# Performance work log

Measured on AMD Instinct MI355X. Metric: run time of the kernel, lower is better.

## Reference

```python
import jax, jax.numpy as jnp
import numpy as np

NS = 0.4      # neighborhood_size
GS = 8        # grid_size
RNN = 128     # rnn_size
EMB = 64      # embedding_size
NMIX = 20     # nmixtures
N = 1024      # num pedestrians


def setup_inputs() -> dict:
    key = jax.random.key(0)
    ks = jax.random.split(key, 14)
    s = 0.05
    return {
        "xoff": jax.random.normal(ks[0], (N, 2)) * s,
        "xabs": jax.random.uniform(ks[1], (N, 2)),
        "h0": jax.random.normal(ks[2], (1, N, RNN)) * 0.1,
        "c0": jax.random.normal(ks[3], (1, N, RNN)) * 0.1,
        "W_emb": jax.random.normal(ks[4], (EMB, 2)) * s,
        "b_emb": jax.random.normal(ks[5], (EMB,)) * s,
        "W_soc": jax.random.normal(ks[6], (EMB, GS * GS * RNN)) * s,
        "b_soc": jax.random.normal(ks[7], (EMB,)) * s,
        "W_ih": jax.random.normal(ks[8], (4 * RNN, 2 * EMB)) * s,
        "W_hh": jax.random.normal(ks[9], (4 * RNN, RNN)) * s,
        "b_ih": jax.random.normal(ks[10], (4 * RNN,)) * s,
        "b_hh": jax.random.normal(ks[11], (4 * RNN,)) * s,
        "W_out": jax.random.normal(ks[12], (6 * NMIX, RNN)) * s,
        "b_out": jax.random.normal(ks[13], (6 * NMIX,)) * s,
    }


def grid_mask(xabs, dtype):
    # Vectorized getGridMask: [N, N, GS*GS] one-hot neighbor binning.
    x, y = xabs[:, 0], xabs[:, 1]
    dx = x[None, :] - (x[:, None] - NS / 2)  # other_x - width_low, [N, N]
    dy = y[None, :] - (y[:, None] - NS / 2)
    cx = jnp.floor(dx / NS * GS).astype(jnp.int32)
    cy = jnp.floor(dy / NS * GS).astype(jnp.int32)
    n = x.shape[0]
    valid = ((dx >= 0) & (dx < NS) & (dy >= 0) & (dy < NS)
             & (cx >= 0) & (cx < GS) & (cy >= 0) & (cy < GS)
             & ~jnp.eye(n, dtype=bool))
    cell = jnp.clip(cx + cy * GS, 0, GS * GS - 1)
    return jax.nn.one_hot(cell, GS * GS, dtype=dtype) * valid[..., None].astype(dtype)


def reference(xoff, xabs, h0, c0, W_emb, b_emb, W_soc, b_soc,
              W_ih, W_hh, b_ih, b_hh, W_out, b_out):
    n = xabs.shape[0]
    # predict_distance=True -> embed offsets
    emb = jax.nn.relu(xoff @ W_emb.T + b_emb)                 # [N, 64]
    grid = grid_mask(xabs, emb.dtype)                          # [N, N, 64]
    h = h0[0]                                                  # [N, 128]
    # getSocialTensor: scatter neighbor hidden states into grid bins
    social = jnp.einsum('nmg,mh->ngh', grid, h).reshape(n, GS * GS * RNN)
    pool = jax.nn.relu(social @ W_soc.T + b_soc)               # [N, 64]
    xin = jnp.concatenate([emb, pool], axis=-1)                # [N, 128]
    # single-step LSTM, torch gate order i, f, g, o
    gates = xin @ W_ih.T + h @ W_hh.T + b_ih + b_hh            # [N, 512]
    i, f, g, o = jnp.split(gates, 4, axis=-1)
    c = jax.nn.sigmoid(f) * c0[0] + jax.nn.sigmoid(i) * jnp.tanh(g)
    hn = jax.nn.sigmoid(o) * jnp.tanh(c)
    out = hn @ W_out.T + b_out                                 # [N, 120]
    mu1, mu2, ls1, ls2, rho, pi_logits = jnp.split(out, 6, axis=1)
    return (mu1, mu2, ls1, ls2, rho, pi_logits)
```

## Files before the change

### kernel.cpp

```cpp
#include <hip/hip_runtime.h>
#include <hip/hip_bf16.h>

#define NN_ 1024

#define U_WGF  0
#define U_SHI  131072
#define U_ACTH 655360
#define U_P    917504
#define F_WOUT 2555904
#define F_HN   2572288

typedef __attribute__((ext_vector_type(8))) short short8;
typedef __attribute__((ext_vector_type(4))) float floatx4;

__device__ __forceinline__ float b2f_(unsigned short u) {
    return __uint_as_float(((unsigned)u) << 16);
}
__device__ __forceinline__ unsigned short f2bu(float f) {
    __hip_bfloat16 b = __float2bfloat16(f);
    return *(unsigned short*)&b;
}
__device__ __forceinline__ float ldin(const void* p, int i, int isbf) {
    return isbf ? b2f_(((const unsigned short*)p)[i]) : ((const float*)p)[i];
}
__device__ __forceinline__ int detect_bf16(const void* Wih, int tid) {
    unsigned wv = ((const unsigned*)Wih)[tid];
    unsigned e8 = (wv >> 7) & 0xFFu;
    return (__syncthreads_count((e8 >= 96u && e8 <= 134u) ? 1 : 0) > 128) ? 1 : 0;
}

__global__ __launch_bounds__(256) void prep_kernel(
        const void* __restrict__ xoff, const void* __restrict__ h0,
        const void* __restrict__ Wsoc, const void* __restrict__ Wemb,
        const void* __restrict__ bemb, const void* __restrict__ Wih,
        const void* __restrict__ Whh,  const void* __restrict__ Wout,
        float* __restrict__ ws) {
    const int tid = threadIdx.x;
    const int isbf = detect_bf16(Wih, tid);
    unsigned short* u = (unsigned short*)ws;
    const int t0 = (blockIdx.x * 256 + tid) * 8;
    unsigned short hv[8];
    if (t0 < 131072) {
        int jl = (t0 >> 3) & 15, q = (t0 >> 7) & 3, kb = (t0 >> 9) & 7, jt = t0 >> 12;
        int j = (jt & 3) * 128 + (jt >> 2) * 16 + jl;
        int k0 = kb * 32 + q * 8;
#pragma unroll
        for (int r = 0; r < 8; r++) {
            int k = k0 + r;
            float v = (k < 128) ? ldin(Wih, j * 128 + k, isbf)
                                : ldin(Whh, j * 128 + (k - 128), isbf);
            hv[r] = f2bu(v);
        }
        *(short8*)(u + U_WGF + t0) = *(short8*)hv;
    } else if (t0 < 147456) {
        int t2 = t0 - 131072; int r = t2 >> 7, j0 = t2 & 127;
#pragma unroll
        for (int i = 0; i < 8; i++) {
            int j = j0 + i;
            ws[F_WOUT + t2 + i] = (j < 120) ? ldin(Wout, j * 128 + r, isbf) : 0.0f;
        }
    } else if (t0 < 671744) {
        int t2 = t0 - 147456;
        int e = (t2 >> 3) & 63, q = (t2 >> 9) & 3, j = (t2 >> 11) & 3, g = t2 >> 13;
        int src = e * 8192 + g * 128 + j * 32 + q * 8;
#pragma unroll
        for (int r = 0; r < 8; r++) hv[r] = f2bu(ldin(Wsoc, src + r, isbf));
        *(short8*)(u + U_SHI + t2) = *(short8*)hv;
    } else if (t0 < 802816) {
        int t2 = t0 - 671744; int n = t2 >> 7, k = t2 & 127;
#pragma unroll
        for (int i = 0; i < 8; i++) hv[i] = f2bu(ldin(h0, t2 + i, isbf));
        *(short8*)(u + U_ACTH + n * 256 + 128 + k) = *(short8*)hv;
    } else {
        int t2 = t0 - 802816; int n = t2 >> 6, e0 = t2 & 63;
        float x0 = ldin(xoff, 2 * n, isbf), x1 = ldin(xoff, 2 * n + 1, isbf);
#pragma unroll
        for (int i = 0; i < 8; i++) {
            int e = e0 + i;
            float v = fmaf(x0, ldin(Wemb, 2 * e, isbf),
                      fmaf(x1, ldin(Wemb, 2 * e + 1, isbf), ldin(bemb, e, isbf)));
            hv[i] = f2bu(fmaxf(v, 0.0f));
        }
        *(short8*)(u + U_ACTH + n * 256 + e0) = *(short8*)hv;
    }
}

__global__ __launch_bounds__(256) void pgemm_kernel(float* __restrict__ ws) {
    const unsigned short* u = (const unsigned short*)ws;
    const short* Ah  = (const short*)(u + U_ACTH);
    const short* Shi = (const short*)(u + U_SHI);
    unsigned short* P16 = (unsigned short*)ws + U_P;
    const int tid = threadIdx.x, lane = tid & 63, wv = tid >> 6;
    const int B_ = blockIdx.y * 64 + blockIdx.x;
    const int mtile = B_ & 63, rest = B_ >> 6;
    const int cg = rest >> 1, thalf = rest & 1;
    const int m = lane & 15, q = lane >> 4;
    const int g = cg * 4 + wv;
    const int abase = (mtile * 16 + m) * 256 + 128 + q * 8;
    short8 ah[4];
#pragma unroll
    for (int j = 0; j < 4; j++) ah[j] = *(const short8*)(Ah + abase + 32 * j);
    const int rowl = mtile * 16 + q * 4;
#pragma unroll
    for (int tt = 0; tt < 2; tt++) {
        const int t = thalf * 2 + tt;
        const int e = t * 16 + m;
        floatx4 c = {0.0f, 0.0f, 0.0f, 0.0f};
#pragma unroll
        for (int j = 0; j < 4; j++) {
            short8 bh = *(const short8*)(Shi + ((g * 4 + j) * 4 + q) * 512 + e * 8);
            c = __builtin_amdgcn_mfma_f32_16x16x32_bf16(ah[j], bh, c, 0, 0, 0);
        }
        const int n0 = cg * 256 + wv * 64 + t * 16;
#pragma unroll
        for (int r = 0; r < 4; r++)
            P16[(rowl + r) * 4096 + n0 + m] = f2bu(c[r]);
    }
}

__global__ __launch_bounds__(256) void pool_kernel(const void* __restrict__ xabs,
                                                   const void* __restrict__ b_soc,
                                                   const void* __restrict__ Wih_det,
                                                   float* __restrict__ ws) {
    __shared__ float xabs_s[2048];
    __shared__ int   off[NN_];
    __shared__ int   cnt_s;
    __shared__ float4 red4[16][16];
    const int tid = threadIdx.x;
    const int isbf = detect_bf16(Wih_det, tid);
    const int n = blockIdx.x;
    unsigned short* u = (unsigned short*)ws;

    for (int i = tid; i < 2048; i += 256) xabs_s[i] = ldin(xabs, i, isbf);
    if (tid == 0) cnt_s = 0;
    __syncthreads();
    {
        float xs = xabs_s[2 * n]     - 0.2f;
        float ys = xabs_s[2 * n + 1] - 0.2f;
        for (int i = tid; i < NN_; i += 256) {
            float dx = xabs_s[2 * i]     - xs;
            float dy = xabs_s[2 * i + 1] - ys;
            int cx = (int)floorf(dx / 0.4f * 8.0f);
            int cy = (int)floorf(dy / 0.4f * 8.0f);
            bool valid = (dx >= 0.0f) && (dx < 0.4f) && (dy >= 0.0f) && (dy < 0.4f)
                      && (cx >= 0) && (cx < 8) && (cy >= 0) && (cy < 8) && (i != n);
            if (valid) {
                int idx = atomicAdd(&cnt_s, 1);
                off[idx] = i * 4096 + ((cy * 8 + cx) << 6);
            }
        }
    }
    __syncthreads();
    {
        const unsigned short* P16 = (const unsigned short*)ws + U_P;
        const int strm = tid >> 4, e4 = tid & 15;
        const int cc = cnt_s;
        float ax = 0.0f, ay = 0.0f, az = 0.0f, aw = 0.0f;
        for (int j = strm; j < cc; j += 16) {
            int o = off[j];
            ushort4 uu = *(const ushort4*)(P16 + o + 4 * e4);
            ax += b2f_(uu.x); ay += b2f_(uu.y); az += b2f_(uu.z); aw += b2f_(uu.w);
        }
        red4[strm][e4] = make_float4(ax, ay, az, aw);
    }
    __syncthreads();
    if (tid < 16) {
        float s[4] = {0.0f, 0.0f, 0.0f, 0.0f};
#pragma unroll
        for (int s16 = 0; s16 < 16; s16++) {
            float4 r = red4[s16][tid];
            s[0] += r.x; s[1] += r.y; s[2] += r.z; s[3] += r.w;
        }
        int e = 4 * tid;
#pragma unroll
        for (int i = 0; i < 4; i++) {
            float v = fmaxf(s[i] + ldin(b_soc, e + i, isbf), 0.0f);
            u[U_ACTH + n * 256 + 64 + e + i] = f2bu(v);
        }
    }
}

__global__ __launch_bounds__(256) void gates_kernel(const void* __restrict__ c0,
                                                    const void* __restrict__ b_ih,
                                                    const void* __restrict__ b_hh,
                                                    const void* __restrict__ Wih_det,
                                                    float* __restrict__ ws) {
    __shared__ float gl[16][68];
    const int tid = threadIdx.x;
    const int isbf = detect_bf16(Wih_det, tid);
    const unsigned short* u = (const unsigned short*)ws;
    const short* Ah = (const short*)(u + U_ACTH);
    const short* Wg = (const short*)(u + U_WGF);
    const int lane = tid & 63, wv = tid >> 6, m = lane & 15, q = lane >> 4;
    const int m0 = blockIdx.x * 16, y = blockIdx.y;
    const int jt = y * 4 + wv;
    floatx4 acc = {0.0f, 0.0f, 0.0f, 0.0f};
#pragma unroll
    for (int kb = 0; kb < 8; kb++) {
        short8 ah = *(const short8*)(Ah + (m0 + m) * 256 + kb * 32 + q * 8);
        short8 b  = *(const short8*)(Wg + (jt * 8 + kb) * 512 + q * 128 + m * 8);
        acc = __builtin_amdgcn_mfma_f32_16x16x32_bf16(ah, b, acc, 0, 0, 0);
    }
    const int jorig = wv * 128 + y * 16 + m;
    const float bias = ldin(b_ih, jorig, isbf) + ldin(b_hh, jorig, isbf);
#pragma unroll
    for (int r = 0; r < 4; r++)
        gl[q * 4 + r][wv * 16 + m] = acc[r] + bias;
    __syncthreads();
    {
        const int a = tid >> 4, rl = tid & 15;
        const int n = m0 + a, rg = y * 16 + rl;
        float iv = gl[a][rl],      fv = gl[a][16 + rl];
        float gv = gl[a][32 + rl], ov = gl[a][48 + rl];
        float si = 1.0f / (1.0f + expf(-iv));
        float sf = 1.0f / (1.0f + expf(-fv));
        float so = 1.0f / (1.0f + expf(-ov));
        float cc = sf * ldin(c0, n * 128 + rg, isbf) + si * tanhf(gv);
        ws[F_HN + n * 128 + rg] = so * tanhf(cc);
    }
}

__global__ __launch_bounds__(256) void pwout_kernel(const void* __restrict__ b_out,
                                                    const void* __restrict__ Wih_det,
                                                    const float* __restrict__ ws,
                                                    float* __restrict__ out) {
    __shared__ __align__(16) float hnl[2][128];
    const int tid = threadIdx.x;
    const int isbf = detect_bf16(Wih_det, tid);
    const int n0 = blockIdx.x * 2;
    const int half = tid >> 7, t2 = tid & 127;
    const int n = n0 + half;
    hnl[half][t2] = ws[F_HN + n * 128 + t2];
    __syncthreads();
    if (t2 < 120) {
        int j = t2;
        float acc = ldin(b_out, j, isbf);
        for (int r = 0; r < 128; r += 4) {
            float4 hq = *(const float4*)&hnl[half][r];
            acc = fmaf(hq.x, ws[F_WOUT + (r + 0) * 128 + j], acc);
            acc = fmaf(hq.y, ws[F_WOUT + (r + 1) * 128 + j], acc);
            acc = fmaf(hq.z, ws[F_WOUT + (r + 2) * 128 + j], acc);
            acc = fmaf(hq.w, ws[F_WOUT + (r + 3) * 128 + j], acc);
        }
        int ch = j / 20, wc = j - ch * 20;
        out[ch * 20480 + n * 20 + wc] = acc;
    }
}

extern "C" void kernel_launch(void* const* d_in, const int* in_sizes, int n_in,
                              void* d_out, int out_size, void* d_ws, size_t ws_size,
                              hipStream_t stream) {
    const void* xoff  = d_in[0];
    const void* xabs  = d_in[1];
    const void* h0    = d_in[2];
    const void* c0    = d_in[3];
    const void* W_emb = d_in[4];
    const void* b_emb = d_in[5];
    const void* W_soc = d_in[6];
    const void* b_soc = d_in[7];
    const void* W_ih  = d_in[8];
    const void* W_hh  = d_in[9];
    const void* b_ih  = d_in[10];
    const void* b_hh  = d_in[11];
    const void* W_out = d_in[12];
    const void* b_out = d_in[13];
    float* ws = (float*)d_ws;
    float* out = (float*)d_out;

    prep_kernel<<<424, 256, 0, stream>>>(xoff, h0, W_soc, W_emb, b_emb,
                                         W_ih, W_hh, W_out, ws);
    pgemm_kernel<<<dim3(64, 32), 256, 0, stream>>>(ws);
    pool_kernel<<<1024, 256, 0, stream>>>(xabs, b_soc, W_ih, ws);
    gates_kernel<<<dim3(64, 8), 256, 0, stream>>>(c0, b_ih, b_hh, W_ih, ws);
    pwout_kernel<<<512, 256, 0, stream>>>(b_out, W_ih, ws, out);
}
```

Measured before the change: 117.9 us.

## Move neighbor binning into prep kernel and fuse gates with output projection

Neighbor-list construction (grid binning of xabs) moves out of pool_kernel into extra blocks of prep_kernel, which write per-pedestrian offset lists and counts to the workspace. pool_kernel then only loads the precomputed list and does the gather-reduce. gates_kernel and pwout_kernel are merged into one gateout_kernel that computes all 512 gates for 8 rows per block, applies the LSTM cell in shared memory and does the output projection, removing one launch and the hn round trip through global memory. The fused kernel wastes half of each MFMA tile, since only 8 of 16 rows are used, and runs only 128 blocks, which may underfill the GPU.

New measurement: 145.8 us. 1.24x slower.

```diff
diff --git a/kernel.cpp b/kernel.cpp
--- a/kernel.cpp
+++ b/kernel.cpp
@@ -8,7 +8,8 @@
 #define U_ACTH 655360
 #define U_P    917504
 #define F_WOUT 2555904
-#define F_HN   2572288
+#define I_OFF  2572288
+#define I_CNT  3620864
 
 typedef __attribute__((ext_vector_type(8))) short short8;
 typedef __attribute__((ext_vector_type(4))) float floatx4;
@@ -30,58 +31,88 @@
 }
 
 __global__ __launch_bounds__(256) void prep_kernel(
-        const void* __restrict__ xoff, const void* __restrict__ h0,
+        const void* __restrict__ xoff, const void* __restrict__ xabs,
+        const void* __restrict__ h0,
         const void* __restrict__ Wsoc, const void* __restrict__ Wemb,
         const void* __restrict__ bemb, const void* __restrict__ Wih,
         const void* __restrict__ Whh,  const void* __restrict__ Wout,
         float* __restrict__ ws) {
     const int tid = threadIdx.x;
+    const int bid = blockIdx.x;
     const int isbf = detect_bf16(Wih, tid);
     unsigned short* u = (unsigned short*)ws;
-    const int t0 = (blockIdx.x * 256 + tid) * 8;
-    unsigned short hv[8];
-    if (t0 < 131072) {
-        int jl = (t0 >> 3) & 15, q = (t0 >> 7) & 3, kb = (t0 >> 9) & 7, jt = t0 >> 12;
-        int j = (jt & 3) * 128 + (jt >> 2) * 16 + jl;
-        int k0 = kb * 32 + q * 8;
-#pragma unroll
-        for (int r = 0; r < 8; r++) {
-            int k = k0 + r;
-            float v = (k < 128) ? ldin(Wih, j * 128 + k, isbf)
-                                : ldin(Whh, j * 128 + (k - 128), isbf);
-            hv[r] = f2bu(v);
-        }
-        *(short8*)(u + U_WGF + t0) = *(short8*)hv;
-    } else if (t0 < 147456) {
-        int t2 = t0 - 131072; int r = t2 >> 7, j0 = t2 & 127;
-#pragma unroll
-        for (int i = 0; i < 8; i++) {
-            int j = j0 + i;
-            ws[F_WOUT + t2 + i] = (j < 120) ? ldin(Wout, j * 128 + r, isbf) : 0.0f;
-        }
-    } else if (t0 < 671744) {
-        int t2 = t0 - 147456;
-        int e = (t2 >> 3) & 63, q = (t2 >> 9) & 3, j = (t2 >> 11) & 3, g = t2 >> 13;
-        int src = e * 8192 + g * 128 + j * 32 + q * 8;
-#pragma unroll
-        for (int r = 0; r < 8; r++) hv[r] = f2bu(ldin(Wsoc, src + r, isbf));
-        *(short8*)(u + U_SHI + t2) = *(short8*)hv;
-    } else if (t0 < 802816) {
-        int t2 = t0 - 671744; int n = t2 >> 7, k = t2 & 127;
-#pragma unroll
-        for (int i = 0; i < 8; i++) hv[i] = f2bu(ldin(h0, t2 + i, isbf));
-        *(short8*)(u + U_ACTH + n * 256 + 128 + k) = *(short8*)hv;
+
+    if (bid < 424) {
+        const int t0 = (bid * 256 + tid) * 8;
+        unsigned short hv[8];
+        if (t0 < 131072) {
+            int jl = (t0 >> 3) & 15, q = (t0 >> 7) & 3, kb = (t0 >> 9) & 7, jt = t0 >> 12;
+            int j = (jt & 3) * 128 + (jt >> 2) * 16 + jl;
+            int k0 = kb * 32 + q * 8;
+#pragma unroll
+            for (int r = 0; r < 8; r++) {
+                int k = k0 + r;
+                float v = (k < 128) ? ldin(Wih, j * 128 + k, isbf)
+                                    : ldin(Whh, j * 128 + (k - 128), isbf);
+                hv[r] = f2bu(v);
+            }
+            *(short8*)(u + U_WGF + t0) = *(short8*)hv;
+        } else if (t0 < 147456) {
+            int t2 = t0 - 131072; int r = t2 >> 7, j0 = t2 & 127;
+#pragma unroll
+            for (int i = 0; i < 8; i++) {
+                int j = j0 + i;
+                ws[F_WOUT + t2 + i] = (j < 120) ? ldin(Wout, j * 128 + r, isbf) : 0.0f;
+            }
+        } else if (t0 < 671744) {
+            int t2 = t0 - 147456;
+            int e = (t2 >> 3) & 63, q = (t2 >> 9) & 3, j = (t2 >> 11) & 3, g = t2 >> 13;
+            int src = e * 8192 + g * 128 + j * 32 + q * 8;
+#pragma unroll
+            for (int r = 0; r < 8; r++) hv[r] = f2bu(ldin(Wsoc, src + r, isbf));
+            *(short8*)(u + U_SHI + t2) = *(short8*)hv;
+        } else if (t0 < 802816) {
+            int t2 = t0 - 671744; int n = t2 >> 7, k = t2 & 127;
+#pragma unroll
+            for (int i = 0; i < 8; i++) hv[i] = f2bu(ldin(h0, t2 + i, isbf));
+            *(short8*)(u + U_ACTH + n * 256 + 128 + k) = *(short8*)hv;
+        } else {
+            int t2 = t0 - 802816; int n = t2 >> 6, e0 = t2 & 63;
+            float x0 = ldin(xoff, 2 * n, isbf), x1 = ldin(xoff, 2 * n + 1, isbf);
+#pragma unroll
+            for (int i = 0; i < 8; i++) {
+                int e = e0 + i;
+                float v = fmaf(x0, ldin(Wemb, 2 * e, isbf),
+                          fmaf(x1, ldin(Wemb, 2 * e + 1, isbf), ldin(bemb, e, isbf)));
+                hv[i] = f2bu(fmaxf(v, 0.0f));
+            }
+            *(short8*)(u + U_ACTH + n * 256 + e0) = *(short8*)hv;
+        }
     } else {
-        int t2 = t0 - 802816; int n = t2 >> 6, e0 = t2 & 63;
-        float x0 = ldin(xoff, 2 * n, isbf), x1 = ldin(xoff, 2 * n + 1, isbf);
-#pragma unroll
-        for (int i = 0; i < 8; i++) {
-            int e = e0 + i;
-            float v = fmaf(x0, ldin(Wemb, 2 * e, isbf),
-                      fmaf(x1, ldin(Wemb, 2 * e + 1, isbf), ldin(bemb, e, isbf)));
-            hv[i] = f2bu(fmaxf(v, 0.0f));
-        }
-        *(short8*)(u + U_ACTH + n * 256 + e0) = *(short8*)hv;
+        __shared__ float xs_[2048];
+        __shared__ int cnt_s[4];
+        for (int i = tid; i < 2048; i += 256) xs_[i] = ldin(xabs, i, isbf);
+        if (tid < 4) cnt_s[tid] = 0;
+        __syncthreads();
+        const int a = tid >> 6, t = tid & 63;
+        const int n = (bid - 424) * 4 + a;
+        unsigned* OFF = (unsigned*)ws + I_OFF + n * 1024;
+        const float xsn = xs_[2 * n]     - 0.2f;
+        const float ysn = xs_[2 * n + 1] - 0.2f;
+        for (int i = t; i < NN_; i += 64) {
+            float dx = xs_[2 * i]     - xsn;
+            float dy = xs_[2 * i + 1] - ysn;
+            int cx = (int)floorf(dx / 0.4f * 8.0f);
+            int cy = (int)floorf(dy / 0.4f * 8.0f);
+            bool valid = (dx >= 0.0f) && (dx < 0.4f) && (dy >= 0.0f) && (dy < 0.4f)
+                      && (cx >= 0) && (cx < 8) && (cy >= 0) && (cy < 8) && (i != n);
+            if (valid) {
+                int pos = atomicAdd(&cnt_s[a], 1);
+                OFF[pos] = (unsigned)(i * 4096 + ((cy * 8 + cx) << 6));
+            }
+        }
+        __syncthreads();
+        if (tid < 4) ((unsigned*)ws)[I_CNT + (bid - 424) * 4 + tid] = (unsigned)cnt_s[tid];
     }
 }
 
@@ -118,46 +149,27 @@
     }
 }
 
-__global__ __launch_bounds__(256) void pool_kernel(const void* __restrict__ xabs,
-                                                   const void* __restrict__ b_soc,
+__global__ __launch_bounds__(256) void pool_kernel(const void* __restrict__ b_soc,
                                                    const void* __restrict__ Wih_det,
                                                    float* __restrict__ ws) {
-    __shared__ float xabs_s[2048];
-    __shared__ int   off[NN_];
-    __shared__ int   cnt_s;
+    __shared__ int off_s[1024];
     __shared__ float4 red4[16][16];
     const int tid = threadIdx.x;
     const int isbf = detect_bf16(Wih_det, tid);
     const int n = blockIdx.x;
     unsigned short* u = (unsigned short*)ws;
-
-    for (int i = tid; i < 2048; i += 256) xabs_s[i] = ldin(xabs, i, isbf);
-    if (tid == 0) cnt_s = 0;
-    __syncthreads();
-    {
-        float xs = xabs_s[2 * n]     - 0.2f;
-        float ys = xabs_s[2 * n + 1] - 0.2f;
-        for (int i = tid; i < NN_; i += 256) {
-            float dx = xabs_s[2 * i]     - xs;
-            float dy = xabs_s[2 * i + 1] - ys;
-            int cx = (int)floorf(dx / 0.4f * 8.0f);
-            int cy = (int)floorf(dy / 0.4f * 8.0f);
-            bool valid = (dx >= 0.0f) && (dx < 0.4f) && (dy >= 0.0f) && (dy < 0.4f)
-                      && (cx >= 0) && (cx < 8) && (cy >= 0) && (cy < 8) && (i != n);
-            if (valid) {
-                int idx = atomicAdd(&cnt_s, 1);
-                off[idx] = i * 4096 + ((cy * 8 + cx) << 6);
-            }
-        }
+    const int cc = (int)((const unsigned*)ws)[I_CNT + n];
+    {
+        const unsigned* lst = (const unsigned*)ws + I_OFF + n * 1024;
+        for (int j = tid; j < cc; j += 256) off_s[j] = (int)lst[j];
     }
     __syncthreads();
     {
         const unsigned short* P16 = (const unsigned short*)ws + U_P;
         const int strm = tid >> 4, e4 = tid & 15;
-        const int cc = cnt_s;
         float ax = 0.0f, ay = 0.0f, az = 0.0f, aw = 0.0f;
         for (int j = strm; j < cc; j += 16) {
-            int o = off[j];
+            int o = off_s[j];
             ushort4 uu = *(const ushort4*)(P16 + o + 4 * e4);
             ax += b2f_(uu.x); ay += b2f_(uu.y); az += b2f_(uu.z); aw += b2f_(uu.w);
         }
@@ -180,70 +192,77 @@
     }
 }
 
-__global__ __launch_bounds__(256) void gates_kernel(const void* __restrict__ c0,
-                                                    const void* __restrict__ b_ih,
-                                                    const void* __restrict__ b_hh,
-                                                    const void* __restrict__ Wih_det,
-                                                    float* __restrict__ ws) {
-    __shared__ float gl[16][68];
+__global__ __launch_bounds__(256) void gateout_kernel(const void* __restrict__ c0,
+                                                      const void* __restrict__ b_ih,
+                                                      const void* __restrict__ b_hh,
+                                                      const void* __restrict__ b_out,
+                                                      const void* __restrict__ Wih_det,
+                                                      const float* __restrict__ ws,
+                                                      float* __restrict__ out) {
+    __shared__ float gl[8][512];
+    __shared__ __align__(16) float hnl[8][128];
     const int tid = threadIdx.x;
     const int isbf = detect_bf16(Wih_det, tid);
     const unsigned short* u = (const unsigned short*)ws;
     const short* Ah = (const short*)(u + U_ACTH);
     const short* Wg = (const short*)(u + U_WGF);
+    const int n0 = blockIdx.x * 8;
     const int lane = tid & 63, wv = tid >> 6, m = lane & 15, q = lane >> 4;
-    const int m0 = blockIdx.x * 16, y = blockIdx.y;
-    const int jt = y * 4 + wv;
-    floatx4 acc = {0.0f, 0.0f, 0.0f, 0.0f};
-#pragma unroll
-    for (int kb = 0; kb < 8; kb++) {
-        short8 ah = *(const short8*)(Ah + (m0 + m) * 256 + kb * 32 + q * 8);
-        short8 b  = *(const short8*)(Wg + (jt * 8 + kb) * 512 + q * 128 + m * 8);
-        acc = __builtin_amdgcn_mfma_f32_16x16x32_bf16(ah, b, acc, 0, 0, 0);
-    }
-    const int jorig = wv * 128 + y * 16 + m;
-    const float bias = ldin(b_ih, jorig, isbf) + ldin(b_hh, jorig, isbf);
-#pragma unroll
-    for (int r = 0; r < 4; r++)
-        gl[q * 4 + r][wv * 16 + m] = acc[r] + bias;
-    __syncthreads();
-    {
-        const int a = tid >> 4, rl = tid & 15;
-        const int n = m0 + a, rg = y * 16 + rl;
-        float iv = gl[a][rl],      fv = gl[a][16 + rl];
-        float gv = gl[a][32 + rl], ov = gl[a][48 + rl];
+
+    {
+        short8 af[8];
+        const short8 z8 = {0, 0, 0, 0, 0, 0, 0, 0};
+#pragma unroll
+        for (int kb = 0; kb < 8; ++kb)
+            af[kb] = (m < 8) ? *(const short8*)(Ah + (n0 + m) * 256 + kb * 32 + q * 8)
+                             : z8;
+#pragma unroll
+        for (int y2 = 0; y2 < 8; ++y2) {
+            floatx4 c = {0.f, 0.f, 0.f, 0.f};
+#pragma unroll
+            for (int kb = 0; kb < 8; ++kb) {
+                short8 b = *(const short8*)(Wg + ((y2 * 4 + wv) * 8 + kb) * 512 + q * 128 + m * 8);
+                c = __builtin_amdgcn_mfma_f32_16x16x32_bf16(af[kb], b, c, 0, 0, 0);
+            }
+            if (q < 2) {
+                const int jor = wv * 128 + y2 * 16 + m;
+                const float bias = ldin(b_ih, jor, isbf) + ldin(b_hh, jor, isbf);
+#pragma unroll
+                for (int r = 0; r < 4; ++r)
+                    gl[q * 4 + r][wv * 128 + y2 * 16 + m] = c[r] + bias;
+            }
+        }
+    }
+    __syncthreads();
+    for (int z = tid; z < 1024; z += 256) {
+        const int a = z >> 7, r = z & 127, n = n0 + a;
+        float iv = gl[a][r],       fv = gl[a][128 + r];
+        float gv = gl[a][256 + r], ov = gl[a][384 + r];
         float si = 1.0f / (1.0f + expf(-iv));
         float sf = 1.0f / (1.0f + expf(-fv));
         float so = 1.0f / (1.0f + expf(-ov));
-        float cc = sf * ldin(c0, n * 128 + rg, isbf) + si * tanhf(gv);
-        ws[F_HN + n * 128 + rg] = so * tanhf(cc);
-    }
-}
-
-__global__ __launch_bounds__(256) void pwout_kernel(const void* __restrict__ b_out,
-                                                    const void* __restrict__ Wih_det,
-                                                    const float* __restrict__ ws,
-                                                    float* __restrict__ out) {
-    __shared__ __align__(16) float hnl[2][128];
-    const int tid = threadIdx.x;
-    const int isbf = detect_bf16(Wih_det, tid);
-    const int n0 = blockIdx.x * 2;
-    const int half = tid >> 7, t2 = tid & 127;
-    const int n = n0 + half;
-    hnl[half][t2] = ws[F_HN + n * 128 + t2];
-    __syncthreads();
-    if (t2 < 120) {
-        int j = t2;
-        float acc = ldin(b_out, j, isbf);
-        for (int r = 0; r < 128; r += 4) {
-            float4 hq = *(const float4*)&hnl[half][r];
-            acc = fmaf(hq.x, ws[F_WOUT + (r + 0) * 128 + j], acc);
-            acc = fmaf(hq.y, ws[F_WOUT + (r + 1) * 128 + j], acc);
-            acc = fmaf(hq.z, ws[F_WOUT + (r + 2) * 128 + j], acc);
-            acc = fmaf(hq.w, ws[F_WOUT + (r + 3) * 128 + j], acc);
-        }
-        int ch = j / 20, wc = j - ch * 20;
-        out[ch * 20480 + n * 20 + wc] = acc;
+        float cc = sf * ldin(c0, n * 128 + r, isbf) + si * tanhf(gv);
+        hnl[a][r] = so * tanhf(cc);
+    }
+    __syncthreads();
+    {
+        const int jj = tid & 127, g2 = tid >> 7;
+        if (jj < 120) {
+            const int ch = jj / 20, wc = jj - ch * 20;
+#pragma unroll
+            for (int ai = 0; ai < 4; ++ai) {
+                const int a = g2 * 4 + ai, n = n0 + a;
+                float acc = ldin(b_out, jj, isbf);
+                for (int r = 0; r < 128; r += 4) {
+                    float4 hq = *(const float4*)&hnl[a][r];
+                    acc = fmaf(hq.x, ws[F_WOUT + (r + 0) * 128 + jj], acc);
+                    acc = fmaf(hq.y, ws[F_WOUT + (r + 1) * 128 + jj], acc);
+                    acc = fmaf(hq.z, ws[F_WOUT + (r + 2) * 128 + jj], acc);
+                    acc = fmaf(hq.w, ws[F_WOUT + (r + 3) * 128 + jj], acc);
+                }
+                out[ch * 20480 + n * 20 + wc] = acc;
+            }
+        }
     }
 }
 
@@ -267,10 +286,9 @@
     float* ws = (float*)d_ws;
     float* out = (float*)d_out;
 
-    prep_kernel<<<424, 256, 0, stream>>>(xoff, h0, W_soc, W_emb, b_emb,
+    prep_kernel<<<680, 256, 0, stream>>>(xoff, xabs, h0, W_soc, W_emb, b_emb,
                                          W_ih, W_hh, W_out, ws);
     pgemm_kernel<<<dim3(64, 32), 256, 0, stream>>>(ws);
-    pool_kernel<<<1024, 256, 0, stream>>>(xabs, b_soc, W_ih, ws);
-    gates_kernel<<<dim3(64, 8), 256, 0, stream>>>(c0, b_ih, b_hh, W_ih, ws);
-    pwout_kernel<<<512, 256, 0, stream>>>(b_out, W_ih, ws, out);
-}
+    pool_kernel<<<1024, 256, 0, stream>>>(b_soc, W_ih, ws);
+    gateout_kernel<<<128, 256, 0, stream>>>(c0, b_ih, b_hh, b_out, W_ih, ws, out);
+}
```

## Move neighbor-list construction from pool kernel into prep kernel blocks

Applied to the files above, without the earlier changes.

The per-pedestrian neighbor binning (grid-cell offsets and count) is now computed by 256 extra blocks of the prep kernel, four pedestrians per block with one wave each, and written to global workspace. The pool kernel only reads the precomputed list and count before doing the gather-reduce. This takes the xabs staging and the binning loop off the pool kernel's critical path and runs them alongside the weight preparation. The cost is extra global writes and reads of the offset lists, plus a larger prep grid.

Result: no change. 117.2 us, median of 2 (-0.5%).

```diff
diff --git a/kernel.cpp b/kernel.cpp
--- a/kernel.cpp
+++ b/kernel.cpp
@@ -9,6 +9,8 @@
 #define U_P    917504
 #define F_WOUT 2555904
 #define F_HN   2572288
+#define I_OFF  2703360
+#define I_CNT  3751936
 
 typedef __attribute__((ext_vector_type(8))) short short8;
 typedef __attribute__((ext_vector_type(4))) float floatx4;
@@ -30,58 +32,88 @@
 }
 
 __global__ __launch_bounds__(256) void prep_kernel(
-        const void* __restrict__ xoff, const void* __restrict__ h0,
+        const void* __restrict__ xoff, const void* __restrict__ xabs,
+        const void* __restrict__ h0,
         const void* __restrict__ Wsoc, const void* __restrict__ Wemb,
         const void* __restrict__ bemb, const void* __restrict__ Wih,
         const void* __restrict__ Whh,  const void* __restrict__ Wout,
         float* __restrict__ ws) {
     const int tid = threadIdx.x;
+    const int bid = blockIdx.x;
     const int isbf = detect_bf16(Wih, tid);
     unsigned short* u = (unsigned short*)ws;
-    const int t0 = (blockIdx.x * 256 + tid) * 8;
-    unsigned short hv[8];
-    if (t0 < 131072) {
-        int jl = (t0 >> 3) & 15, q = (t0 >> 7) & 3, kb = (t0 >> 9) & 7, jt = t0 >> 12;
-        int j = (jt & 3) * 128 + (jt >> 2) * 16 + jl;
-        int k0 = kb * 32 + q * 8;
-#pragma unroll
-        for (int r = 0; r < 8; r++) {
-            int k = k0 + r;
-            float v = (k < 128) ? ldin(Wih, j * 128 + k, isbf)
-                                : ldin(Whh, j * 128 + (k - 128), isbf);
-            hv[r] = f2bu(v);
-        }
-        *(short8*)(u + U_WGF + t0) = *(short8*)hv;
-    } else if (t0 < 147456) {
-        int t2 = t0 - 131072; int r = t2 >> 7, j0 = t2 & 127;
-#pragma unroll
-        for (int i = 0; i < 8; i++) {
-            int j = j0 + i;
-            ws[F_WOUT + t2 + i] = (j < 120) ? ldin(Wout, j * 128 + r, isbf) : 0.0f;
-        }
-    } else if (t0 < 671744) {
-        int t2 = t0 - 147456;
-        int e = (t2 >> 3) & 63, q = (t2 >> 9) & 3, j = (t2 >> 11) & 3, g = t2 >> 13;
-        int src = e * 8192 + g * 128 + j * 32 + q * 8;
-#pragma unroll
-        for (int r = 0; r < 8; r++) hv[r] = f2bu(ldin(Wsoc, src + r, isbf));
-        *(short8*)(u + U_SHI + t2) = *(short8*)hv;
-    } else if (t0 < 802816) {
-        int t2 = t0 - 671744; int n = t2 >> 7, k = t2 & 127;
-#pragma unroll
-        for (int i = 0; i < 8; i++) hv[i] = f2bu(ldin(h0, t2 + i, isbf));
-        *(short8*)(u + U_ACTH + n * 256 + 128 + k) = *(short8*)hv;
+
+    if (bid < 424) {
+        const int t0 = (bid * 256 + tid) * 8;
+        unsigned short hv[8];
+        if (t0 < 131072) {
+            int jl = (t0 >> 3) & 15, q = (t0 >> 7) & 3, kb = (t0 >> 9) & 7, jt = t0 >> 12;
+            int j = (jt & 3) * 128 + (jt >> 2) * 16 + jl;
+            int k0 = kb * 32 + q * 8;
+#pragma unroll
+            for (int r = 0; r < 8; r++) {
+                int k = k0 + r;
+                float v = (k < 128) ? ldin(Wih, j * 128 + k, isbf)
+                                    : ldin(Whh, j * 128 + (k - 128), isbf);
+                hv[r] = f2bu(v);
+            }
+            *(short8*)(u + U_WGF + t0) = *(short8*)hv;
+        } else if (t0 < 147456) {
+            int t2 = t0 - 131072; int r = t2 >> 7, j0 = t2 & 127;
+#pragma unroll
+            for (int i = 0; i < 8; i++) {
+                int j = j0 + i;
+                ws[F_WOUT + t2 + i] = (j < 120) ? ldin(Wout, j * 128 + r, isbf) : 0.0f;
+            }
+        } else if (t0 < 671744) {
+            int t2 = t0 - 147456;
+            int e = (t2 >> 3) & 63, q = (t2 >> 9) & 3, j = (t2 >> 11) & 3, g = t2 >> 13;
+            int src = e * 8192 + g * 128 + j * 32 + q * 8;
+#pragma unroll
+            for (int r = 0; r < 8; r++) hv[r] = f2bu(ldin(Wsoc, src + r, isbf));
+            *(short8*)(u + U_SHI + t2) = *(short8*)hv;
+        } else if (t0 < 802816) {
+            int t2 = t0 - 671744; int n = t2 >> 7, k = t2 & 127;
+#pragma unroll
+            for (int i = 0; i < 8; i++) hv[i] = f2bu(ldin(h0, t2 + i, isbf));
+            *(short8*)(u + U_ACTH + n * 256 + 128 + k) = *(short8*)hv;
+        } else {
+            int t2 = t0 - 802816; int n = t2 >> 6, e0 = t2 & 63;
+            float x0 = ldin(xoff, 2 * n, isbf), x1 = ldin(xoff, 2 * n + 1, isbf);
+#pragma unroll
+            for (int i = 0; i < 8; i++) {
+                int e = e0 + i;
+                float v = fmaf(x0, ldin(Wemb, 2 * e, isbf),
+                          fmaf(x1, ldin(Wemb, 2 * e + 1, isbf), ldin(bemb, e, isbf)));
+                hv[i] = f2bu(fmaxf(v, 0.0f));
+            }
+            *(short8*)(u + U_ACTH + n * 256 + e0) = *(short8*)hv;
+        }
     } else {
-        int t2 = t0 - 802816; int n = t2 >> 6, e0 = t2 & 63;
-        float x0 = ldin(xoff, 2 * n, isbf), x1 = ldin(xoff, 2 * n + 1, isbf);
-#pragma unroll
-        for (int i = 0; i < 8; i++) {
-            int e = e0 + i;
-            float v = fmaf(x0, ldin(Wemb, 2 * e, isbf),
-                      fmaf(x1, ldin(Wemb, 2 * e + 1, isbf), ldin(bemb, e, isbf)));
-            hv[i] = f2bu(fmaxf(v, 0.0f));
-        }
-        *(short8*)(u + U_ACTH + n * 256 + e0) = *(short8*)hv;
+        __shared__ float xs_[2048];
+        __shared__ int cnt_s[4];
+        for (int i = tid; i < 2048; i += 256) xs_[i] = ldin(xabs, i, isbf);
+        if (tid < 4) cnt_s[tid] = 0;
+        __syncthreads();
+        const int a = tid >> 6, t = tid & 63;
+        const int n = (bid - 424) * 4 + a;
+        unsigned* OFF = (unsigned*)ws + I_OFF + n * 1024;
+        const float xsn = xs_[2 * n]     - 0.2f;
+        const float ysn = xs_[2 * n + 1] - 0.2f;
+        for (int i = t; i < NN_; i += 64) {
+            float dx = xs_[2 * i]     - xsn;
+            float dy = xs_[2 * i + 1] - ysn;
+            int cx = (int)floorf(dx / 0.4f * 8.0f);
+            int cy = (int)floorf(dy / 0.4f * 8.0f);
+            bool valid = (dx >= 0.0f) && (dx < 0.4f) && (dy >= 0.0f) && (dy < 0.4f)
+                      && (cx >= 0) && (cx < 8) && (cy >= 0) && (cy < 8) && (i != n);
+            if (valid) {
+                int pos = atomicAdd(&cnt_s[a], 1);
+                OFF[pos] = (unsigned)(i * 4096 + ((cy * 8 + cx) << 6));
+            }
+        }
+        __syncthreads();
+        if (tid < 4) ((unsigned*)ws)[I_CNT + (bid - 424) * 4 + tid] = (unsigned)cnt_s[tid];
     }
 }
 
@@ -118,46 +150,27 @@
     }
 }
 
-__global__ __launch_bounds__(256) void pool_kernel(const void* __restrict__ xabs,
-                                                   const void* __restrict__ b_soc,
+__global__ __launch_bounds__(256) void pool_kernel(const void* __restrict__ b_soc,
                                                    const void* __restrict__ Wih_det,
                                                    float* __restrict__ ws) {
-    __shared__ float xabs_s[2048];
-    __shared__ int   off[NN_];
-    __shared__ int   cnt_s;
+    __shared__ int off_s[1024];
     __shared__ float4 red4[16][16];
     const int tid = threadIdx.x;
     const int isbf = detect_bf16(Wih_det, tid);
     const int n = blockIdx.x;
     unsigned short* u = (unsigned short*)ws;
-
-    for (int i = tid; i < 2048; i += 256) xabs_s[i] = ldin(xabs, i, isbf);
-    if (tid == 0) cnt_s = 0;
-    __syncthreads();
+    const int cc = (int)((const unsigned*)ws)[I_CNT + n];
     {
-        float xs = xabs_s[2 * n]     - 0.2f;
-        float ys = xabs_s[2 * n + 1] - 0.2f;
-        for (int i = tid; i < NN_; i += 256) {
-            float dx = xabs_s[2 * i]     - xs;
-            float dy = xabs_s[2 * i + 1] - ys;
-            int cx = (int)floorf(dx / 0.4f * 8.0f);
-            int cy = (int)floorf(dy / 0.4f * 8.0f);
-            bool valid = (dx >= 0.0f) && (dx < 0.4f) && (dy >= 0.0f) && (dy < 0.4f)
-                      && (cx >= 0) && (cx < 8) && (cy >= 0) && (cy < 8) && (i != n);
-            if (valid) {
-                int idx = atomicAdd(&cnt_s, 1);
-                off[idx] = i * 4096 + ((cy * 8 + cx) << 6);
-            }
-        }
+        const unsigned* lst = (const unsigned*)ws + I_OFF + n * 1024;
+        for (int j = tid; j < cc; j += 256) off_s[j] = (int)lst[j];
     }
     __syncthreads();
     {
         const unsigned short* P16 = (const unsigned short*)ws + U_P;
         const int strm = tid >> 4, e4 = tid & 15;
-        const int cc = cnt_s;
         float ax = 0.0f, ay = 0.0f, az = 0.0f, aw = 0.0f;
         for (int j = strm; j < cc; j += 16) {
-            int o = off[j];
+            int o = off_s[j];
             ushort4 uu = *(const ushort4*)(P16 + o + 4 * e4);
             ax += b2f_(uu.x); ay += b2f_(uu.y); az += b2f_(uu.z); aw += b2f_(uu.w);
         }
@@ -267,10 +280,10 @@
     float* ws = (float*)d_ws;
     float* out = (float*)d_out;
 
-    prep_kernel<<<424, 256, 0, stream>>>(xoff, h0, W_soc, W_emb, b_emb,
+    prep_kernel<<<680, 256, 0, stream>>>(xoff, xabs, h0, W_soc, W_emb, b_emb,
                                          W_ih, W_hh, W_out, ws);
     pgemm_kernel<<<dim3(64, 32), 256, 0, stream>>>(ws);
-    pool_kernel<<<1024, 256, 0, stream>>>(xabs, b_soc, W_ih, ws);
+    pool_kernel<<<1024, 256, 0, stream>>>(b_soc, W_ih, ws);
     gates_kernel<<<dim3(64, 8), 256, 0, stream>>>(c0, b_ih, b_hh, W_ih, ws);
     pwout_kernel<<<512, 256, 0, stream>>>(b_out, W_ih, ws, out);
 }
```
